# Kernel optimization log

Hardware: AMD Instinct MI355X
Metric: run time of the kernel (lower is better)

The kernel has to match this reference:

```python
import jax, jax.numpy as jnp
import numpy as np

HIDDEN_DIM = 512


def setup_inputs() -> dict:
    key = jax.random.key(0)
    ks = jax.random.split(key, 7)
    B, SQ, SKV, DIN, H = 8, 2048, 2048, 1024, HIDDEN_DIM
    query = jax.random.normal(ks[0], (B, SQ, H), dtype=jnp.float32)
    states = jax.random.normal(ks[1], (B, SKV, DIN), dtype=jnp.float32)
    mask = jax.random.uniform(ks[2], (B, SQ, SKV), dtype=jnp.float32)
    # LazyLinear params (stored as [in, out]; torch uses x @ W.T with W [out, in])
    Wk = jax.random.normal(ks[3], (DIN, H), dtype=jnp.float32) * (1.0 / np.sqrt(DIN))
    bk = jax.random.normal(ks[4], (H,), dtype=jnp.float32) * 0.02
    Wv = jax.random.normal(ks[5], (DIN, H), dtype=jnp.float32) * (1.0 / np.sqrt(DIN))
    bv = jax.random.normal(ks[6], (H,), dtype=jnp.float32) * 0.02
    return {"query": query, "states": states, "mask": mask,
            "Wk": Wk, "bk": bk, "Wv": Wv, "bv": bv}


def reference(query, states, mask, Wk, bk, Wv, bv):
    # transform_states=True: project states into key/value spaces
    keys = states @ Wk + bk        # [B, S_kv, H]
    values = states @ Wv + bv      # [B, S_kv, H]
    # bmm(query, keys^T) / sqrt(H)
    scale = 1.0 / jnp.sqrt(jnp.asarray(keys.shape[-1], dtype=query.dtype))
    scores = jnp.einsum('bqh,bkh->bqk', query, keys) * scale  # [B, S_q, S_kv]
    scores = mask * scores  # multiplicative mask
    # source detaches the softmax output
    attn = jax.lax.stop_gradient(jax.nn.softmax(scores, axis=-1))
    return jnp.einsum('bqk,bkh->bqh', attn, values)  # [B, S_q, H]
```

## Files before the change

### kernel.cpp

```cpp
#include <hip/hip_runtime.h>
#include <hip/hip_bf16.h>
#include <stdint.h>

#define BM 128
#define BN 128
#define BK 32

typedef __bf16 bf16;
typedef bf16 bf16x4 __attribute__((ext_vector_type(4)));
typedef bf16 bf16x8 __attribute__((ext_vector_type(8)));
typedef float f32x4 __attribute__((ext_vector_type(4)));

typedef const __attribute__((address_space(1))) void* gas1_t;
typedef __attribute__((address_space(3))) void* las3_t;

__device__ __forceinline__ void gl_lds16(const void* g, void* l) {
  __builtin_amdgcn_global_load_lds((gas1_t)g, (las3_t)l, 16, 0, 0);
}

__device__ __forceinline__ void gemm_core(const bf16* A, const bf16* Bt,
                                          int lda, int ldb, int kTiles,
                                          bf16* As, bf16* Bs, f32x4 acc[4][4]) {
  const int tid = threadIdx.x;
  const int lane = tid & 63;
  const int wid = tid >> 6;
  const int wr = wid >> 1, wc = wid & 1;
  const int lr = lane & 15, lg = lane >> 4;

  for (int kt = 0; kt < kTiles; ++kt) {
    const bf16* Ak = A + kt * BK;
    const bf16* Bk = Bt + kt * BK;
#pragma unroll
    for (int p = 0; p < 2; ++p) {
      int c = p * 256 + tid;
      int row = c >> 2, k8 = (c & 3) << 3;
      gl_lds16(Ak + (size_t)row * lda + k8, As + c * 8);
      gl_lds16(Bk + (size_t)row * ldb + k8, Bs + c * 8);
    }
    __syncthreads();
    bf16x8 af[4], bfr[4];
#pragma unroll
    for (int i = 0; i < 4; ++i) {
      af[i]  = *(const bf16x8*)(As + (wr * 64 + i * 16 + lr) * BK + lg * 8);
      bfr[i] = *(const bf16x8*)(Bs + (wc * 64 + i * 16 + lr) * BK + lg * 8);
    }
#pragma unroll
    for (int i = 0; i < 4; ++i)
#pragma unroll
      for (int j = 0; j < 4; ++j)
        acc[i][j] = __builtin_amdgcn_mfma_f32_16x16x32_bf16(af[i], bfr[j], acc[i][j], 0, 0, 0);
    __syncthreads();
  }
}

__global__ __launch_bounds__(256) void k_cast2(const float* __restrict__ a,
                                               bf16* __restrict__ oa, int na8,
                                               const float* __restrict__ b,
                                               bf16* __restrict__ ob, int nb8) {
  int i = blockIdx.x * blockDim.x + threadIdx.x;
  int stride = gridDim.x * blockDim.x;
  int ntot = na8 + nb8;
  for (; i < ntot; i += stride) {
    const float* src = (i < na8) ? a : b;
    bf16* dst = (i < na8) ? oa : ob;
    int idx = (i < na8) ? i : i - na8;
    float4 x = ((const float4*)src)[2 * (size_t)idx];
    float4 y = ((const float4*)src)[2 * (size_t)idx + 1];
    bf16x8 o;
    o[0] = (bf16)x.x; o[1] = (bf16)x.y; o[2] = (bf16)x.z; o[3] = (bf16)x.w;
    o[4] = (bf16)y.x; o[5] = (bf16)y.y; o[6] = (bf16)y.z; o[7] = (bf16)y.w;
    ((bf16x8*)dst)[idx] = o;
  }
}

__global__ __launch_bounds__(256) void k_transposeW(const float* __restrict__ Wk,
                                                    const float* __restrict__ Wv,
                                                    bf16* __restrict__ WT) {
  __shared__ float t[32][33];
  const float* W = blockIdx.z ? Wv : Wk;
  bf16* O = WT + (size_t)blockIdx.z * 512 * 1024;
  int h0 = blockIdx.x * 32, d0 = blockIdx.y * 32;
  int tx = threadIdx.x & 31, ty = threadIdx.x >> 5;
#pragma unroll
  for (int yy = 0; yy < 4; ++yy)
    t[ty + yy * 8][tx] = W[(size_t)(d0 + ty + yy * 8) * 512 + h0 + tx];
  __syncthreads();
#pragma unroll
  for (int yy = 0; yy < 4; ++yy)
    O[(size_t)(h0 + ty + yy * 8) * 1024 + d0 + tx] = (bf16)t[tx][ty + yy * 8];
}

__global__ __launch_bounds__(256) void k_proj(const bf16* __restrict__ WT,
                                              const bf16* __restrict__ S,
                                              const float* __restrict__ bk,
                                              const float* __restrict__ bv,
                                              bf16* __restrict__ Kb,
                                              bf16* __restrict__ VT) {
  __shared__ bf16 As[BM * BK], Bs[BN * BK];
  f32x4 acc[4][4] = {};
  int h0 = blockIdx.x * BM, t0 = blockIdx.y * BN;
  const int lane = threadIdx.x & 63, wid = threadIdx.x >> 6;
  const int wr = wid >> 1, wc = wid & 1, lr = lane & 15, lg = lane >> 4;
  if (blockIdx.z == 0) {
    gemm_core(WT + (size_t)h0 * 1024, S + (size_t)t0 * 1024, 1024, 1024, 1024 / BK, As, Bs, acc);
#pragma unroll
    for (int i = 0; i < 4; ++i) {
      int hb = h0 + wr * 64 + i * 16 + lg * 4;
      float4 bias = *(const float4*)(bk + hb);
#pragma unroll
      for (int j = 0; j < 4; ++j) {
        int t = t0 + wc * 64 + j * 16 + lr;
        f32x4 v = acc[i][j];
        bf16x4 o;
        o[0] = (bf16)(v[0] + bias.x); o[1] = (bf16)(v[1] + bias.y);
        o[2] = (bf16)(v[2] + bias.z); o[3] = (bf16)(v[3] + bias.w);
        *(bf16x4*)(Kb + (size_t)t * 512 + hb) = o;
      }
    }
  } else {
    gemm_core(S + (size_t)t0 * 1024, WT + (size_t)(512 + h0) * 1024, 1024, 1024, 1024 / BK, As, Bs, acc);
#pragma unroll
    for (int i = 0; i < 4; ++i) {
      int tb = t0 + wr * 64 + i * 16 + lg * 4;
      int b = tb >> 11, s = tb & 2047;
#pragma unroll
      for (int j = 0; j < 4; ++j) {
        int h = h0 + wc * 64 + j * 16 + lr;
        float bias = bv[h];
        f32x4 v = acc[i][j];
        bf16x4 o;
        o[0] = (bf16)(v[0] + bias); o[1] = (bf16)(v[1] + bias);
        o[2] = (bf16)(v[2] + bias); o[3] = (bf16)(v[3] + bias);
        *(bf16x4*)(VT + ((size_t)(b * 512 + h)) * 2048 + s) = o;
      }
    }
  }
}

__global__ __launch_bounds__(256) void k_scores(const bf16* __restrict__ Kb,
                                                const bf16* __restrict__ Qb,
                                                const float* __restrict__ mask,
                                                bf16* __restrict__ P,
                                                float* __restrict__ lsum) {
  __shared__ bf16 As[BM * BK], Bs[BN * BK];
  f32x4 acc[4][4] = {};
  float4 mreg[16];
  const int b = blockIdx.z;
  const int kv0 = blockIdx.x * BM, q0 = blockIdx.y * BN;
  const bf16* A  = Kb + (size_t)b * 2048 * 512 + (size_t)kv0 * 512;
  const bf16* Bt = Qb + (size_t)b * 2048 * 512 + (size_t)q0 * 512;
  const float* Mb = mask + (size_t)b * 2048 * 2048;
  const int tid = threadIdx.x, lane = tid & 63, wid = tid >> 6;
  const int wr = wid >> 1, wc = wid & 1, lr = lane & 15, lg = lane >> 4;
#pragma unroll
  for (int kt = 0; kt < 16; ++kt) {
#pragma unroll
    for (int p = 0; p < 2; ++p) {
      int c = p * 256 + tid;
      int row = c >> 2, k8 = (c & 3) << 3;
      gl_lds16(A + (size_t)row * 512 + kt * BK + k8, As + c * 8);
      gl_lds16(Bt + (size_t)row * 512 + kt * BK + k8, Bs + c * 8);
    }
    {
      int q = q0 + wc * 64 + (kt >> 2) * 16 + lr;
      int kvb = kv0 + wr * 64 + (kt & 3) * 16 + lg * 4;
      mreg[kt] = *(const float4*)(Mb + (size_t)q * 2048 + kvb);
    }
    __syncthreads();
    bf16x8 af[4], bfr[4];
#pragma unroll
    for (int i = 0; i < 4; ++i) {
      af[i]  = *(const bf16x8*)(As + (wr * 64 + i * 16 + lr) * BK + lg * 8);
      bfr[i] = *(const bf16x8*)(Bs + (wc * 64 + i * 16 + lr) * BK + lg * 8);
    }
#pragma unroll
    for (int i = 0; i < 4; ++i)
#pragma unroll
      for (int j = 0; j < 4; ++j)
        acc[i][j] = __builtin_amdgcn_mfma_f32_16x16x32_bf16(af[i], bfr[j], acc[i][j], 0, 0, 0);
    __syncthreads();
  }
  const float scale = 0.04419417382415922f;
  bf16* Pb = P + (size_t)b * 2048 * 2048;
  float rs[4] = {0.f, 0.f, 0.f, 0.f};
#pragma unroll
  for (int j = 0; j < 4; ++j) {
    int q = q0 + wc * 64 + j * 16 + lr;
    size_t qrow = (size_t)q * 2048;
#pragma unroll
    for (int i = 0; i < 4; ++i) {
      int kvb = kv0 + wr * 64 + i * 16 + lg * 4;
      float4 m4 = mreg[j * 4 + i];
      f32x4 v = acc[i][j];
      float p0 = __expf(v[0] * scale * m4.x);
      float p1 = __expf(v[1] * scale * m4.y);
      float p2 = __expf(v[2] * scale * m4.z);
      float p3 = __expf(v[3] * scale * m4.w);
      bf16x4 o; o[0] = (bf16)p0; o[1] = (bf16)p1; o[2] = (bf16)p2; o[3] = (bf16)p3;
      *(bf16x4*)(Pb + qrow + kvb) = o;
      rs[j] += p0 + p1 + p2 + p3;
    }
  }
#pragma unroll
  for (int j = 0; j < 4; ++j) {
    float v = rs[j];
    v += __shfl_xor(v, 16);
    v += __shfl_xor(v, 32);
    if (lane < 16)
      atomicAdd(&lsum[b * 2048 + q0 + wc * 64 + j * 16 + lr], v);
  }
}

__global__ __launch_bounds__(256) void k_pv(const bf16* __restrict__ VT,
                                            const bf16* __restrict__ P,
                                            const float* __restrict__ lsum,
                                            float* __restrict__ out) {
  __shared__ bf16 As[BM * BK], Bs[BN * BK];
  f32x4 acc[4][4] = {};
  int b = blockIdx.z;
  int h0 = blockIdx.x * BM, q0 = blockIdx.y * BN;
  gemm_core(VT + (size_t)b * 512 * 2048 + (size_t)h0 * 2048,
            P + (size_t)b * 2048 * 2048 + (size_t)q0 * 2048, 2048, 2048, 2048 / BK, As, Bs, acc);
  float* Ob = out + (size_t)b * 2048 * 512;
  const float* lb = lsum + b * 2048;
  const int lane = threadIdx.x & 63, wid = threadIdx.x >> 6;
  const int wr = wid >> 1, wc = wid & 1, lr = lane & 15, lg = lane >> 4;
#pragma unroll
  for (int j = 0; j < 4; ++j) {
    int q = q0 + wc * 64 + j * 16 + lr;
    float inv = 1.0f / lb[q];
#pragma unroll
    for (int i = 0; i < 4; ++i) {
      int hb = h0 + wr * 64 + i * 16 + lg * 4;
      f32x4 v = acc[i][j];
      float4 o4 = make_float4(v[0] * inv, v[1] * inv, v[2] * inv, v[3] * inv);
      *(float4*)(Ob + (size_t)q * 512 + hb) = o4;
    }
  }
}

extern "C" void kernel_launch(void* const* d_in, const int* in_sizes, int n_in,
                              void* d_out, int out_size, void* d_ws, size_t ws_size,
                              hipStream_t stream) {
  const float* query  = (const float*)d_in[0];
  const float* states = (const float*)d_in[1];
  const float* mask   = (const float*)d_in[2];
  const float* Wk     = (const float*)d_in[3];
  const float* bk     = (const float*)d_in[4];
  const float* Wv     = (const float*)d_in[5];
  const float* bv     = (const float*)d_in[6];
  float* out = (float*)d_out;

  char* ws = (char*)d_ws;
  bf16* WT = (bf16*)(ws);
  bf16* Qb = (bf16*)(ws + (2ull << 20));
  bf16* Kb = (bf16*)(ws + (18ull << 20));
  bf16* VT = (bf16*)(ws + (34ull << 20));
  bf16* Sb = (bf16*)(ws + (50ull << 20));
  bf16* P  = (bf16*)(ws + (50ull << 20));
  float* ls = (float*)(ws + (114ull << 20));

  hipMemsetAsync(ls, 0, 8 * 2048 * sizeof(float), stream);
  k_transposeW<<<dim3(16, 32, 2), 256, 0, stream>>>(Wk, Wv, WT);
  k_cast2<<<dim3(3072), 256, 0, stream>>>(states, Sb, 16384 * 1024 / 8,
                                          query, Qb, 8 * 2048 * 512 / 8);
  k_proj<<<dim3(4, 128, 2), 256, 0, stream>>>(WT, Sb, bk, bv, Kb, VT);
  k_scores<<<dim3(16, 16, 8), 256, 0, stream>>>(Kb, Qb, mask, P, ls);
  k_pv<<<dim3(4, 16, 8), 256, 0, stream>>>(VT, P, ls, out);
}
```

Baseline: 451.8 us.

## Double-buffer LDS tiles to prefetch next K-slice during MFMA compute

The shared GEMM core and the scores kernel now use two LDS buffers. The next K tile (and, in the scores kernel, the next mask fragment) is issued with global_load_lds before the current tile is consumed, so global-to-LDS traffic can overlap with the LDS reads and MFMA work, and one barrier per iteration is removed. Wave priority is raised around the MFMA block with s_setprio. In exchange, LDS use per block doubles to 32 KB, which may limit how many blocks fit on a CU. The overlap is also bounded because the end-of-iteration barrier still waits for the outstanding loads.

```diff
diff --git a/kernel.cpp b/kernel.cpp
--- a/kernel.cpp
+++ b/kernel.cpp
@@ -16,6 +16,20 @@
 
 __device__ __forceinline__ void gl_lds16(const void* g, void* l) {
   __builtin_amdgcn_global_load_lds((gas1_t)g, (las3_t)l, 16, 0, 0);
+}
+
+__device__ __forceinline__ void stage_tile(const bf16* A, const bf16* Bt,
+                                           int lda, int ldb, int kt,
+                                           bf16* As, bf16* Bs, int buf) {
+  const int tid = threadIdx.x;
+#pragma unroll
+  for (int p = 0; p < 2; ++p) {
+    int c = p * 256 + tid;
+    int row = c >> 2, k8 = (c & 3) << 3;
+    int off = buf * (BM * BK) + c * 8;
+    gl_lds16(A + (size_t)row * lda + kt * BK + k8, As + off);
+    gl_lds16(Bt + (size_t)row * ldb + kt * BK + k8, Bs + off);
+  }
 }
 
 __device__ __forceinline__ void gemm_core(const bf16* A, const bf16* Bt,
@@ -27,29 +41,29 @@
   const int wr = wid >> 1, wc = wid & 1;
   const int lr = lane & 15, lg = lane >> 4;
 
+  stage_tile(A, Bt, lda, ldb, 0, As, Bs, 0);
+  __syncthreads();
+  int cur = 0;
   for (int kt = 0; kt < kTiles; ++kt) {
-    const bf16* Ak = A + kt * BK;
-    const bf16* Bk = Bt + kt * BK;
-#pragma unroll
-    for (int p = 0; p < 2; ++p) {
-      int c = p * 256 + tid;
-      int row = c >> 2, k8 = (c & 3) << 3;
-      gl_lds16(Ak + (size_t)row * lda + k8, As + c * 8);
-      gl_lds16(Bk + (size_t)row * ldb + k8, Bs + c * 8);
-    }
-    __syncthreads();
+    if (kt + 1 < kTiles)
+      stage_tile(A, Bt, lda, ldb, kt + 1, As, Bs, cur ^ 1);
+    const bf16* Ab = As + cur * (BM * BK);
+    const bf16* Bb = Bs + cur * (BM * BK);
     bf16x8 af[4], bfr[4];
 #pragma unroll
     for (int i = 0; i < 4; ++i) {
-      af[i]  = *(const bf16x8*)(As + (wr * 64 + i * 16 + lr) * BK + lg * 8);
-      bfr[i] = *(const bf16x8*)(Bs + (wc * 64 + i * 16 + lr) * BK + lg * 8);
-    }
+      af[i]  = *(const bf16x8*)(Ab + (wr * 64 + i * 16 + lr) * BK + lg * 8);
+      bfr[i] = *(const bf16x8*)(Bb + (wc * 64 + i * 16 + lr) * BK + lg * 8);
+    }
+    __builtin_amdgcn_s_setprio(1);
 #pragma unroll
     for (int i = 0; i < 4; ++i)
 #pragma unroll
       for (int j = 0; j < 4; ++j)
         acc[i][j] = __builtin_amdgcn_mfma_f32_16x16x32_bf16(af[i], bfr[j], acc[i][j], 0, 0, 0);
+    __builtin_amdgcn_s_setprio(0);
     __syncthreads();
+    cur ^= 1;
   }
 }
 
@@ -96,7 +110,7 @@
                                               const float* __restrict__ bv,
                                               bf16* __restrict__ Kb,
                                               bf16* __restrict__ VT) {
-  __shared__ bf16 As[BM * BK], Bs[BN * BK];
+  __shared__ bf16 As[2 * BM * BK], Bs[2 * BN * BK];
   f32x4 acc[4][4] = {};
   int h0 = blockIdx.x * BM, t0 = blockIdx.y * BN;
   const int lane = threadIdx.x & 63, wid = threadIdx.x >> 6;
@@ -142,7 +156,7 @@
                                                 const float* __restrict__ mask,
                                                 bf16* __restrict__ P,
                                                 float* __restrict__ lsum) {
-  __shared__ bf16 As[BM * BK], Bs[BN * BK];
+  __shared__ bf16 As[2 * BM * BK], Bs[2 * BN * BK];
   f32x4 acc[4][4] = {};
   float4 mreg[16];
   const int b = blockIdx.z;
@@ -152,32 +166,39 @@
   const float* Mb = mask + (size_t)b * 2048 * 2048;
   const int tid = threadIdx.x, lane = tid & 63, wid = tid >> 6;
   const int wr = wid >> 1, wc = wid & 1, lr = lane & 15, lg = lane >> 4;
+
+  stage_tile(A, Bt, 512, 512, 0, As, Bs, 0);
+  {
+    int q = q0 + wc * 64 + lr;
+    int kvb = kv0 + wr * 64 + lg * 4;
+    mreg[0] = *(const float4*)(Mb + (size_t)q * 2048 + kvb);
+  }
+  __syncthreads();
 #pragma unroll
   for (int kt = 0; kt < 16; ++kt) {
-#pragma unroll
-    for (int p = 0; p < 2; ++p) {
-      int c = p * 256 + tid;
-      int row = c >> 2, k8 = (c & 3) << 3;
-      gl_lds16(A + (size_t)row * 512 + kt * BK + k8, As + c * 8);
-      gl_lds16(Bt + (size_t)row * 512 + kt * BK + k8, Bs + c * 8);
-    }
-    {
-      int q = q0 + wc * 64 + (kt >> 2) * 16 + lr;
-      int kvb = kv0 + wr * 64 + (kt & 3) * 16 + lg * 4;
-      mreg[kt] = *(const float4*)(Mb + (size_t)q * 2048 + kvb);
-    }
-    __syncthreads();
+    const int buf = kt & 1;
+    if (kt < 15) {
+      stage_tile(A, Bt, 512, 512, kt + 1, As, Bs, buf ^ 1);
+      const int kn = kt + 1;
+      int q = q0 + wc * 64 + (kn >> 2) * 16 + lr;
+      int kvb = kv0 + wr * 64 + (kn & 3) * 16 + lg * 4;
+      mreg[kn] = *(const float4*)(Mb + (size_t)q * 2048 + kvb);
+    }
+    const bf16* Ab = As + buf * (BM * BK);
+    const bf16* Bb = Bs + buf * (BM * BK);
     bf16x8 af[4], bfr[4];
 #pragma unroll
     for (int i = 0; i < 4; ++i) {
-      af[i]  = *(const bf16x8*)(As + (wr * 64 + i * 16 + lr) * BK + lg * 8);
-      bfr[i] = *(const bf16x8*)(Bs + (wc * 64 + i * 16 + lr) * BK + lg * 8);
-    }
+      af[i]  = *(const bf16x8*)(Ab + (wr * 64 + i * 16 + lr) * BK + lg * 8);
+      bfr[i] = *(const bf16x8*)(Bb + (wc * 64 + i * 16 + lr) * BK + lg * 8);
+    }
+    __builtin_amdgcn_s_setprio(1);
 #pragma unroll
     for (int i = 0; i < 4; ++i)
 #pragma unroll
       for (int j = 0; j < 4; ++j)
         acc[i][j] = __builtin_amdgcn_mfma_f32_16x16x32_bf16(af[i], bfr[j], acc[i][j], 0, 0, 0);
+    __builtin_amdgcn_s_setprio(0);
     __syncthreads();
   }
   const float scale = 0.04419417382415922f;
@@ -215,7 +236,7 @@
                                             const bf16* __restrict__ P,
                                             const float* __restrict__ lsum,
                                             float* __restrict__ out) {
-  __shared__ bf16 As[BM * BK], Bs[BN * BK];
+  __shared__ bf16 As[2 * BM * BK], Bs[2 * BN * BK];
   f32x4 acc[4][4] = {};
   int b = blockIdx.z;
   int h0 = blockIdx.x * BM, q0 = blockIdx.y * BN;
```

New measurement: 462.4 us. 1.02x slower.
